# Performance work log

Hardware: AMD Instinct MI355X
Metric: run time of the kernel (lower is better)

Reference implementation:

```python
import jax, jax.numpy as jnp
import numpy as np

N_HEAD = 16


def setup_inputs() -> dict:
    key = jax.random.key(0)
    k1, k2, k3 = jax.random.split(key, 3)
    B, T, C = 2, 2048, 1024
    x = jax.random.normal(k1, (B, T, C), dtype=jnp.float32)
    w_attn = jax.random.normal(k2, (C, 3 * C), dtype=jnp.float32) * 0.02
    w_proj = jax.random.normal(k3, (C, C), dtype=jnp.float32) * 0.02
    return {"x": x, "w_attn": w_attn, "w_proj": w_proj}


def reference(x, w_attn, w_proj):
    B, T, C = x.shape
    H = N_HEAD
    D = C // H
    qkv = x @ w_attn  # [B, T, 3C]
    q, k, v = jnp.split(qkv, 3, axis=2)
    q = q.reshape(B, T, H, D)
    k = k.reshape(B, T, H, D)
    v = v.reshape(B, T, H, D)
    scale = 1.0 / jnp.sqrt(jnp.asarray(D, dtype=x.dtype))
    # Full T x T score matrix, matching the 'standard_attention' path.
    att = jnp.einsum('bthd,bshd->bhts', q, k) * scale  # [B, H, T, T]
    causal = jnp.tril(jnp.ones((T, T), dtype=bool))
    att = jnp.where(causal[None, None, :, :], att, jnp.asarray(-jnp.inf, dtype=att.dtype))
    att = jax.nn.softmax(att, axis=-1)
    # dropout_p is False (== 0.0) in the original module, so no dropout applied.
    y = jnp.einsum('bhts,bshd->bthd', att, v)  # [B, T, H, D]
    y = y.reshape(B, T, C)
    return y @ w_proj
```

## Files before the change

kernel.cpp:

```cpp
#include <hip/hip_runtime.h>
#include <hip/hip_bf16.h>
#include <math.h>

#define BB 2
#define TT 2048
#define HH 16
#define DD 64
#define CC 1024
#define C3 3072

typedef __attribute__((ext_vector_type(8))) short bf16x8;
typedef __attribute__((ext_vector_type(4))) short bf16x4;
typedef __attribute__((ext_vector_type(4))) float f32x4;
typedef __attribute__((ext_vector_type(2))) unsigned int u32x2;

__device__ __forceinline__ unsigned short f2bf(float f) {
  union { float f; unsigned u; } v; v.f = f;
  unsigned r = v.u + 0x7fffu + ((v.u >> 16) & 1u);
  return (unsigned short)(r >> 16);
}
__device__ __forceinline__ unsigned pack2bf(float a, float b) {
  __hip_bfloat162 h = __float22bfloat162_rn(make_float2(a, b));
  union { __hip_bfloat162 h; unsigned u; } cv; cv.h = h;
  return cv.u;
}

__device__ __forceinline__ void async_cp16(const void* g, void* l) {
  __builtin_amdgcn_global_load_lds(
      (const __attribute__((address_space(1))) void*)g,
      (__attribute__((address_space(3))) void*)l, 16, 0, 0);
}

__global__ __launch_bounds__(256)
void prep(const float* __restrict__ x, const float* __restrict__ w_attn,
          const float* __restrict__ w_proj, unsigned short* __restrict__ xb,
          unsigned short* __restrict__ wat, unsigned short* __restrict__ wpt) {
  __shared__ __align__(16) float Ts[64][68];
  const int bx = blockIdx.x, tid = threadIdx.x;
  if (bx < 1024) {
    int i = bx * 256 + tid;
#pragma unroll
    for (int it = 0; it < 4; ++it, i += 262144) {
      const float4 v = ((const float4*)x)[i];
      bf16x4 o = {(short)f2bf(v.x), (short)f2bf(v.y),
                  (short)f2bf(v.z), (short)f2bf(v.w)};
      ((bf16x4*)xb)[i] = o;
    }
    return;
  }
  const float* W;
  unsigned short* WT;
  int Nd, bound, n0, k0;
  float s;
  if (bx < 1792) {
    const int bid = bx - 1024;
    W = w_attn; WT = wat; Nd = 3072; bound = 1024; s = 0.18033688f;
    n0 = (bid % 48) * 64; k0 = (bid / 48) * 64;
  } else {
    const int bid = bx - 1792;
    W = w_proj; WT = wpt; Nd = 1024; bound = 0; s = 1.0f;
    n0 = (bid % 16) * 64; k0 = (bid / 16) * 64;
  }
  const int rl = tid >> 4, c4 = tid & 15;
#pragma unroll
  for (int it = 0; it < 4; ++it) {
    const int r = it * 16 + rl;
    *(float4*)&Ts[r][c4 * 4] =
        *(const float4*)(W + (size_t)(k0 + r) * Nd + n0 + c4 * 4);
  }
  __syncthreads();
#pragma unroll
  for (int it = 0; it < 4; ++it) {
    const int n = it * 16 + rl;
    const float sc = (n0 + n < bound) ? s : 1.0f;
    bf16x4 o = {(short)f2bf(Ts[c4 * 4 + 0][n] * sc),
                (short)f2bf(Ts[c4 * 4 + 1][n] * sc),
                (short)f2bf(Ts[c4 * 4 + 2][n] * sc),
                (short)f2bf(Ts[c4 * 4 + 3][n] * sc)};
    *(bf16x4*)(WT + (size_t)(n0 + n) * CC + k0 + c4 * 4) = o;
  }
}

__global__ __launch_bounds__(256, 3)
void gemm_qkv(const unsigned short* __restrict__ A,
              const unsigned short* __restrict__ BT,
              unsigned short* __restrict__ Cb,
              unsigned short* __restrict__ Vout) {
  __shared__ __align__(16) unsigned short As[2 * 128 * 32];
  __shared__ __align__(16) unsigned short Bs[2 * 128 * 32];

  const int tid = threadIdx.x;
  const int w = tid >> 6, lane = tid & 63;
  const int l15 = lane & 15, quad = lane >> 4;
  const int wm = w >> 1, wn = w & 1;
  const int row0 = blockIdx.y * 128, col0 = blockIdx.x * 128;

  const int ca0 = tid, ca1 = tid + 256;
  const int ra0 = ca0 >> 2, ka0 = ((ca0 & 3) ^ ((ca0 >> 3) & 3)) * 8;
  const int ra1 = ca1 >> 2, ka1 = ((ca1 & 3) ^ ((ca1 >> 3) & 3)) * 8;
  const unsigned short* gA0 = A + (size_t)(row0 + ra0) * CC + ka0;
  const unsigned short* gA1 = A + (size_t)(row0 + ra1) * CC + ka1;
  const unsigned short* gB0 = BT + (size_t)(col0 + ra0) * CC + ka0;
  const unsigned short* gB1 = BT + (size_t)(col0 + ra1) * CC + ka1;
  const int la0 = tid * 16, la1 = tid * 16 + 4096;

  const int fro = l15 * 64 + 16 * (quad ^ ((l15 >> 1) & 3));

  f32x4 acc[4][4];
#pragma unroll
  for (int i = 0; i < 4; ++i)
#pragma unroll
    for (int j = 0; j < 4; ++j) acc[i][j] = (f32x4){0.f, 0.f, 0.f, 0.f};

  async_cp16(gA0, (char*)As + la0);
  async_cp16(gA1, (char*)As + la1);
  async_cp16(gB0, (char*)Bs + la0);
  async_cp16(gB1, (char*)Bs + la1);

  for (int i = 0; i < 32; ++i) {
    const int cur = i & 1;
    __syncthreads();

    if (i + 1 < 32) {
      const int k1 = (i + 1) * 32;
      const int ab = (cur ^ 1) * 8192;
      async_cp16(gA0 + k1, (char*)As + ab + la0);
      async_cp16(gA1 + k1, (char*)As + ab + la1);
      async_cp16(gB0 + k1, (char*)Bs + ab + la0);
      async_cp16(gB1 + k1, (char*)Bs + ab + la1);
    }

    const char* fA = (const char*)As + cur * 8192 + wm * 4096 + fro;
    const char* fB = (const char*)Bs + cur * 8192 + wn * 4096 + fro;

    bf16x8 af[4], bf[4];
#pragma unroll
    for (int mt = 0; mt < 4; ++mt) af[mt] = *(const bf16x8*)(fA + mt * 1024);
#pragma unroll
    for (int nt = 0; nt < 4; ++nt) bf[nt] = *(const bf16x8*)(fB + nt * 1024);
#pragma unroll
    for (int mt = 0; mt < 4; ++mt)
#pragma unroll
      for (int nt = 0; nt < 4; ++nt)
        acc[mt][nt] = __builtin_amdgcn_mfma_f32_16x16x32_bf16(
            af[mt], bf[nt], acc[mt][nt], 0, 0, 0);
  }

  if (col0 >= 2048) {
#pragma unroll
    for (int mt = 0; mt < 4; ++mt) {
      const int rbase = row0 + wm * 64 + mt * 16 + quad * 4;
      const int bq = rbase >> 11, t0 = rbase & 2047;
#pragma unroll
      for (int nt = 0; nt < 4; ++nt) {
        const int d = col0 + wn * 64 + nt * 16 + l15 - 2048;
        bf16x4 o = {(short)f2bf(acc[mt][nt][0]), (short)f2bf(acc[mt][nt][1]),
                    (short)f2bf(acc[mt][nt][2]), (short)f2bf(acc[mt][nt][3])};
        *(bf16x4*)(Vout + (((size_t)(bq << 10) + d) << 11) + t0) = o;
      }
    }
  } else {
#pragma unroll
    for (int mt = 0; mt < 4; ++mt) {
      const int rbase = row0 + wm * 64 + mt * 16 + quad * 4;
#pragma unroll
      for (int r = 0; r < 4; ++r) {
        unsigned short* cr =
            Cb + (size_t)(rbase + r) * C3 + col0 + wn * 64 + l15;
#pragma unroll
        for (int nt = 0; nt < 4; ++nt) cr[nt * 16] = f2bf(acc[mt][nt][r]);
      }
    }
  }
}

__global__ __launch_bounds__(256, 2)
void gemm_out(const unsigned short* __restrict__ A,
              const unsigned short* __restrict__ BT,
              float* __restrict__ Cf) {
  __shared__ __align__(16) unsigned short As[2 * 64 * 64];
  __shared__ __align__(16) unsigned short Bs[2 * 128 * 64];

  const int tid = threadIdx.x;
  const int w = tid >> 6, lane = tid & 63;
  const int l15 = lane & 15, quad = lane >> 4;
  const int wm = w >> 1, wn = w & 1;
  const int row0 = blockIdx.y * 64, col0 = blockIdx.x * 128;

  const int ca0 = tid, ca1 = tid + 256;
  const int ra0 = ca0 >> 3, ka0 = ((ca0 & 7) ^ ((ca0 >> 3) & 7)) * 8;
  const int ra1 = ca1 >> 3, ka1 = ((ca1 & 7) ^ ((ca1 >> 3) & 7)) * 8;
  const unsigned short* gA0 = A + (size_t)(row0 + ra0) * CC + ka0;
  const unsigned short* gA1 = A + (size_t)(row0 + ra1) * CC + ka1;
  const unsigned short* gB[4];
  int lb[4];
#pragma unroll
  for (int t = 0; t < 4; ++t) {
    const int c = tid + t * 256;
    const int rb = c >> 3, kb = ((c & 7) ^ ((c >> 3) & 7)) * 8;
    gB[t] = BT + (size_t)(col0 + rb) * CC + kb;
    lb[t] = c * 16;
  }
  const int la0 = tid * 16, la1 = tid * 16 + 4096;

  const int fro = l15 * 128 + ((quad ^ (l15 & 7)) << 4);

  f32x4 acc[2][4];
#pragma unroll
  for (int i = 0; i < 2; ++i)
#pragma unroll
    for (int j = 0; j < 4; ++j) acc[i][j] = (f32x4){0.f, 0.f, 0.f, 0.f};

  async_cp16(gA0, (char*)As + la0);
  async_cp16(gA1, (char*)As + la1);
#pragma unroll
  for (int t = 0; t < 4; ++t) async_cp16(gB[t], (char*)Bs + lb[t]);

  for (int i = 0; i < 16; ++i) {
    const int cur = i & 1;
    __syncthreads();

    if (i + 1 < 16) {
      const int k1 = (i + 1) * 64;
      const int ab = (cur ^ 1) * 8192, bb = (cur ^ 1) * 16384;
      async_cp16(gA0 + k1, (char*)As + ab + la0);
      async_cp16(gA1 + k1, (char*)As + ab + la1);
#pragma unroll
      for (int t = 0; t < 4; ++t) async_cp16(gB[t] + k1, (char*)Bs + bb + lb[t]);
    }

    const char* fA = (const char*)As + cur * 8192 + wm * 4096 + fro;
    const char* fB = (const char*)Bs + cur * 16384 + wn * 8192 + fro;

#pragma unroll
    for (int kh = 0; kh < 2; ++kh) {
      const int xo = kh * 64;
      bf16x8 af[2], bf[4];
#pragma unroll
      for (int mt = 0; mt < 2; ++mt)
        af[mt] = *(const bf16x8*)(fA + mt * 2048 + ((fro + xo) & 127) - (fro & 127));
#pragma unroll
      for (int nt = 0; nt < 4; ++nt)
        bf[nt] = *(const bf16x8*)(fB + nt * 2048 + ((fro + xo) & 127) - (fro & 127));
#pragma unroll
      for (int mt = 0; mt < 2; ++mt)
#pragma unroll
        for (int nt = 0; nt < 4; ++nt)
          acc[mt][nt] = __builtin_amdgcn_mfma_f32_16x16x32_bf16(
              af[mt], bf[nt], acc[mt][nt], 0, 0, 0);
    }
  }

#pragma unroll
  for (int mt = 0; mt < 2; ++mt) {
    const int rbase = row0 + wm * 32 + mt * 16 + quad * 4;
#pragma unroll
    for (int r = 0; r < 4; ++r) {
      float* cr = Cf + (size_t)(rbase + r) * CC + col0 + wn * 64 + l15;
#pragma unroll
      for (int nt = 0; nt < 4; ++nt) cr[nt * 16] = acc[mt][nt][r];
    }
  }
}

__device__ __forceinline__ void attn_chunk(
    const int c, const int qt, const int l15, const int quad,
    const bf16x8 (&kf)[2][2], const bf16x8 (&qf)[4][2], const bf16x8 onesf,
    const unsigned short* __restrict__ vbase, char* psw, const int psrow,
    f32x4 (&O)[4][4], f32x4 (&lacc)[4]) {
  bf16x8 vf[4];
#pragma unroll
  for (int dt = 0; dt < 4; ++dt)
    vf[dt] = *(const bf16x8*)(vbase + (size_t)dt * 16 * TT + 32 * c);

  f32x4 S[2][4];
#pragma unroll
  for (int ks = 0; ks < 2; ++ks)
#pragma unroll
    for (int qs = 0; qs < 4; ++qs) {
      f32x4 z = (f32x4){-12.f, -12.f, -12.f, -12.f};
      z = __builtin_amdgcn_mfma_f32_16x16x32_bf16(kf[ks][0], qf[qs][0], z, 0, 0, 0);
      z = __builtin_amdgcn_mfma_f32_16x16x32_bf16(kf[ks][1], qf[qs][1], z, 0, 0, 0);
      S[ks][qs] = z;
    }

  if (c >= 2 * qt) {
#pragma unroll
    for (int ks = 0; ks < 2; ++ks)
#pragma unroll
      for (int qs = 0; qs < 4; ++qs)
#pragma unroll
        for (int r = 0; r < 4; ++r)
          if (32 * c + ks * 16 + quad * 4 + r > qt * 64 + qs * 16 + l15)
            S[ks][qs][r] = -INFINITY;
  }

#pragma unroll
  for (int ks = 0; ks < 2; ++ks)
#pragma unroll
    for (int qs = 0; qs < 4; ++qs) {
      u32x2 d;
      d[0] = pack2bf(__builtin_amdgcn_exp2f(S[ks][qs][0]),
                     __builtin_amdgcn_exp2f(S[ks][qs][1]));
      d[1] = pack2bf(__builtin_amdgcn_exp2f(S[ks][qs][2]),
                     __builtin_amdgcn_exp2f(S[ks][qs][3]));
      *(u32x2*)(psw + qs * 2304 + psrow + (((ks + l15) & 3) << 5) + quad * 8) = d;
    }

#pragma unroll
  for (int qs = 0; qs < 4; ++qs) {
    const bf16x8 pf = *(const bf16x8*)(psw + qs * 2304 + psrow +
                                       ((((quad >> 1) + l15) & 3) << 5) +
                                       ((quad & 1) << 4));
    lacc[qs] = __builtin_amdgcn_mfma_f32_16x16x32_bf16(onesf, pf, lacc[qs], 0, 0, 0);
#pragma unroll
    for (int dt = 0; dt < 4; ++dt)
      O[dt][qs] = __builtin_amdgcn_mfma_f32_16x16x32_bf16(vf[dt], pf, O[dt][qs], 0, 0, 0);
  }
}

#define LOADK(dst, cc)                                                   \
  do {                                                                   \
    const unsigned short* kp = kbase + (size_t)(32 * (cc)) * C3;         \
    dst[0][0] = *(const bf16x8*)(kp);                                    \
    dst[0][1] = *(const bf16x8*)(kp + 32);                               \
    dst[1][0] = *(const bf16x8*)(kp + 16 * C3);                          \
    dst[1][1] = *(const bf16x8*)(kp + 16 * C3 + 32);                     \
  } while (0)

__global__ __launch_bounds__(256, 2)
void attn_mfma(const unsigned short* __restrict__ qkvb,
               const unsigned short* __restrict__ vt,
               unsigned short* __restrict__ y) {
  const int n = blockIdx.x;
  const int bh = (n & 7) + 8 * ((n >> 3) & 3);
  const int qpair = n >> 5;
  const int b = bh >> 4, h = bh & 15;
  const int tid = threadIdx.x;
  const int w = tid >> 6;
  const int lane = tid & 63;
  const int l15 = lane & 15, quad = lane >> 4;

  __shared__ __align__(16) unsigned short Ps[4 * 4 * 16 * 72];
  __shared__ __align__(16) float Red[2][16][256];
  __shared__ float Red2[2][4][16];

  char* psw = (char*)Ps + w * (4 * 2304);
  const int psrow = l15 * 144;
  const int epoff = l15 * 64 + ((quad ^ (l15 & 3)) << 4);

  const unsigned short* kbase =
      qkvb + (size_t)(b * TT + l15) * C3 + 1024 + h * DD + quad * 8;
  const unsigned short* vbase =
      vt + (size_t)(bh * DD + l15) * TT + quad * 8;

  bf16x8 onesf;
#pragma unroll
  for (int jj = 0; jj < 8; ++jj) onesf[jj] = (short)0x3F80;

  for (int phase = 0; phase < 2; ++phase) {
    const int qt = phase ? qpair : 31 - qpair;
    const int nc = 2 * (qt + 1);

    const unsigned short* qbase =
        qkvb + (size_t)(b * TT + qt * 64 + l15) * C3 + h * DD + quad * 8;
    bf16x8 qf[4][2];
#pragma unroll
    for (int qs = 0; qs < 4; ++qs)
#pragma unroll
      for (int kh = 0; kh < 2; ++kh)
        qf[qs][kh] = *(const bf16x8*)(qbase + qs * 16 * C3 + kh * 32);

    f32x4 O[4][4];
    f32x4 lacc[4];
#pragma unroll
    for (int dt = 0; dt < 4; ++dt)
#pragma unroll
      for (int qs = 0; qs < 4; ++qs) O[dt][qs] = (f32x4){0.f, 0.f, 0.f, 0.f};
#pragma unroll
    for (int qs = 0; qs < 4; ++qs) lacc[qs] = (f32x4){0.f, 0.f, 0.f, 0.f};

    bf16x8 kfA[2][2], kfB[2][2];
    int c = w;
    if (c < nc) {
      LOADK(kfA, c);
      while (true) {
        int cn = c + 4;
        if (cn < nc) LOADK(kfB, cn);
        attn_chunk(c, qt, l15, quad, kfA, qf, onesf, vbase, psw, psrow, O, lacc);
        c = cn;
        if (c >= nc) break;
        cn = c + 4;
        if (cn < nc) LOADK(kfA, cn);
        attn_chunk(c, qt, l15, quad, kfB, qf, onesf, vbase, psw, psrow, O, lacc);
        c = cn;
        if (c >= nc) break;
      }
    }

    __syncthreads();
    if (w & 1) {
      char* rs = (char*)Red + (w >> 1) * 16384;
#pragma unroll
      for (int dt = 0; dt < 4; ++dt)
#pragma unroll
        for (int qs = 0; qs < 4; ++qs)
          *(f32x4*)(rs + (dt * 4 + qs) * 1024 + epoff) = O[dt][qs];
      if (quad == 0) {
#pragma unroll
        for (int qs = 0; qs < 4; ++qs) Red2[w >> 1][qs][l15] = lacc[qs][0];
      }
    }
    __syncthreads();
    float lsum[4];
#pragma unroll
    for (int qs = 0; qs < 4; ++qs) lsum[qs] = lacc[qs][0];
    if (!(w & 1)) {
      char* rs = (char*)Red + (w >> 1) * 16384;
#pragma unroll
      for (int dt = 0; dt < 4; ++dt)
#pragma unroll
        for (int qs = 0; qs < 4; ++qs)
          O[dt][qs] += *(const f32x4*)(rs + (dt * 4 + qs) * 1024 + epoff);
#pragma unroll
      for (int qs = 0; qs < 4; ++qs) lsum[qs] += Red2[w >> 1][qs][l15];
    }
    __syncthreads();
    if (w == 2) {
      char* rs = (char*)Red;
#pragma unroll
      for (int dt = 0; dt < 4; ++dt)
#pragma unroll
        for (int qs = 0; qs < 4; ++qs)
          *(f32x4*)(rs + (dt * 4 + qs) * 1024 + epoff) = O[dt][qs];
      if (quad == 0) {
#pragma unroll
        for (int qs = 0; qs < 4; ++qs) Red2[0][qs][l15] = lsum[qs];
      }
    }
    __syncthreads();
    if (w == 0) {
      char* rs = (char*)Red;
#pragma unroll
      for (int dt = 0; dt < 4; ++dt)
#pragma unroll
        for (int qs = 0; qs < 4; ++qs)
          O[dt][qs] += *(const f32x4*)(rs + (dt * 4 + qs) * 1024 + epoff);
      unsigned short* yr =
          y + (size_t)(b * TT + qt * 64 + l15) * CC + h * DD + quad * 4;
#pragma unroll
      for (int qs = 0; qs < 4; ++qs) {
        const float inv = 1.0f / (lsum[qs] + Red2[0][qs][l15]);
#pragma unroll
        for (int dt = 0; dt < 4; ++dt) {
          bf16x4 o = {(short)f2bf(O[dt][qs][0] * inv),
                      (short)f2bf(O[dt][qs][1] * inv),
                      (short)f2bf(O[dt][qs][2] * inv),
                      (short)f2bf(O[dt][qs][3] * inv)};
          *(bf16x4*)(yr + (size_t)qs * 16 * CC + dt * 16) = o;
        }
      }
    }
  }
}

extern "C" void kernel_launch(void* const* d_in, const int* in_sizes, int n_in,
                              void* d_out, int out_size, void* d_ws,
                              size_t ws_size, hipStream_t stream) {
  const float* x      = (const float*)d_in[0];
  const float* w_attn = (const float*)d_in[1];
  const float* w_proj = (const float*)d_in[2];
  float* out = (float*)d_out;

  unsigned short* xb   = (unsigned short*)d_ws;
  unsigned short* wat  = xb + (size_t)4096 * 1024;
  unsigned short* wpt  = wat + (size_t)3072 * 1024;
  unsigned short* qkvb = wpt + (size_t)1024 * 1024;
  unsigned short* vt   = qkvb + (size_t)4096 * 3072;
  unsigned short* yb   = vt + (size_t)BB * HH * DD * TT;

  dim3 blk(256);

  prep<<<2048, blk, 0, stream>>>(x, w_attn, w_proj, xb, wat, wpt);

  gemm_qkv<<<dim3(C3 / 128, (BB * TT) / 128), blk, 0, stream>>>(
      xb, wat, qkvb, vt);

  attn_mfma<<<dim3(512, 1, 1), blk, 0, stream>>>(qkvb, vt, yb);

  gemm_out<<<dim3(CC / 128, (BB * TT) / 64), blk, 0, stream>>>(yb, wpt, out);
}
```

Measured before the change: 173.8 us.

## Software-pipeline attention chunks: overlap next QK/exp with current PV MFMA

```diff
diff --git a/kernel.cpp b/kernel.cpp
--- a/kernel.cpp
+++ b/kernel.cpp
@@ -263,17 +263,10 @@
   }
 }
 
-__device__ __forceinline__ void attn_chunk(
+__device__ __forceinline__ void s_exp_pack(
     const int c, const int qt, const int l15, const int quad,
-    const bf16x8 (&kf)[2][2], const bf16x8 (&qf)[4][2], const bf16x8 onesf,
-    const unsigned short* __restrict__ vbase, char* psw, const int psrow,
-    f32x4 (&O)[4][4], f32x4 (&lacc)[4]) {
-  bf16x8 vf[4];
-#pragma unroll
-  for (int dt = 0; dt < 4; ++dt)
-    vf[dt] = *(const bf16x8*)(vbase + (size_t)dt * 16 * TT + 32 * c);
-
-  f32x4 S[2][4];
+    const bf16x8 (&kf)[2][2], const bf16x8 (&qf)[4][2],
+    unsigned (&P)[4][4]) {
 #pragma unroll
   for (int ks = 0; ks < 2; ++ks)
 #pragma unroll
@@ -281,32 +274,36 @@
       f32x4 z = (f32x4){-12.f, -12.f, -12.f, -12.f};
       z = __builtin_amdgcn_mfma_f32_16x16x32_bf16(kf[ks][0], qf[qs][0], z, 0, 0, 0);
       z = __builtin_amdgcn_mfma_f32_16x16x32_bf16(kf[ks][1], qf[qs][1], z, 0, 0, 0);
-      S[ks][qs] = z;
-    }
-
-  if (c >= 2 * qt) {
-#pragma unroll
-    for (int ks = 0; ks < 2; ++ks)
-#pragma unroll
-      for (int qs = 0; qs < 4; ++qs)
+      if (c >= 2 * qt) {
 #pragma unroll
         for (int r = 0; r < 4; ++r)
           if (32 * c + ks * 16 + quad * 4 + r > qt * 64 + qs * 16 + l15)
-            S[ks][qs][r] = -INFINITY;
-  }
-
+            z[r] = -INFINITY;
+      }
+      P[qs][2 * ks + 0] = pack2bf(__builtin_amdgcn_exp2f(z[0]),
+                                  __builtin_amdgcn_exp2f(z[1]));
+      P[qs][2 * ks + 1] = pack2bf(__builtin_amdgcn_exp2f(z[2]),
+                                  __builtin_amdgcn_exp2f(z[3]));
+    }
+}
+
+__device__ __forceinline__ void p_write(char* psw, const int psrow,
+                                        const int l15, const int quad,
+                                        const unsigned (&P)[4][4]) {
 #pragma unroll
   for (int ks = 0; ks < 2; ++ks)
 #pragma unroll
     for (int qs = 0; qs < 4; ++qs) {
-      u32x2 d;
-      d[0] = pack2bf(__builtin_amdgcn_exp2f(S[ks][qs][0]),
-                     __builtin_amdgcn_exp2f(S[ks][qs][1]));
-      d[1] = pack2bf(__builtin_amdgcn_exp2f(S[ks][qs][2]),
-                     __builtin_amdgcn_exp2f(S[ks][qs][3]));
+      u32x2 d = {P[qs][2 * ks + 0], P[qs][2 * ks + 1]};
       *(u32x2*)(psw + qs * 2304 + psrow + (((ks + l15) & 3) << 5) + quad * 8) = d;
     }
-
+}
+
+__device__ __forceinline__ void pv_accum(
+    const int l15, const int quad, const bf16x8 onesf,
+    const bf16x8 (&vf)[4], char* psw, const int psrow,
+    f32x4 (&O)[4][4], f32x4 (&lacc)[4]) {
+  __builtin_amdgcn_s_setprio(1);
 #pragma unroll
   for (int qs = 0; qs < 4; ++qs) {
     const bf16x8 pf = *(const bf16x8*)(psw + qs * 2304 + psrow +
@@ -317,6 +314,7 @@
     for (int dt = 0; dt < 4; ++dt)
       O[dt][qs] = __builtin_amdgcn_mfma_f32_16x16x32_bf16(vf[dt], pf, O[dt][qs], 0, 0, 0);
   }
+  __builtin_amdgcn_s_setprio(0);
 }
 
 #define LOADK(dst, cc)                                                   \
@@ -326,6 +324,15 @@
     dst[0][1] = *(const bf16x8*)(kp + 32);                               \
     dst[1][0] = *(const bf16x8*)(kp + 16 * C3);                          \
     dst[1][1] = *(const bf16x8*)(kp + 16 * C3 + 32);                     \
+  } while (0)
+
+#define LOADV(dst, cc)                                                   \
+  do {                                                                   \
+    const unsigned short* vp = vbase + 32 * (cc);                        \
+    dst[0] = *(const bf16x8*)(vp);                                       \
+    dst[1] = *(const bf16x8*)(vp + 16 * TT);                             \
+    dst[2] = *(const bf16x8*)(vp + 32 * TT);                             \
+    dst[3] = *(const bf16x8*)(vp + 48 * TT);                             \
   } while (0)
 
 __global__ __launch_bounds__(256, 2)
@@ -380,20 +387,28 @@
 #pragma unroll
     for (int qs = 0; qs < 4; ++qs) lacc[qs] = (f32x4){0.f, 0.f, 0.f, 0.f};
 
-    bf16x8 kfA[2][2], kfB[2][2];
     int c = w;
     if (c < nc) {
-      LOADK(kfA, c);
+      bf16x8 kX[2][2], kY[2][2], vf[4];
+      unsigned PX[4][4], PY[4][4];
+      LOADK(kX, c);
+      LOADV(vf, c);
+      if (c + 4 < nc) LOADK(kY, c + 4);
+      s_exp_pack(c, qt, l15, quad, kX, qf, PX);
       while (true) {
-        int cn = c + 4;
-        if (cn < nc) LOADK(kfB, cn);
-        attn_chunk(c, qt, l15, quad, kfA, qf, onesf, vbase, psw, psrow, O, lacc);
-        c = cn;
+        p_write(psw, psrow, l15, quad, PX);
+        if (c + 8 < nc) LOADK(kX, c + 8);
+        if (c + 4 < nc) s_exp_pack(c + 4, qt, l15, quad, kY, qf, PY);
+        pv_accum(l15, quad, onesf, vf, psw, psrow, O, lacc);
+        if (c + 4 < nc) LOADV(vf, c + 4);
+        c += 4;
         if (c >= nc) break;
-        cn = c + 4;
-        if (cn < nc) LOADK(kfA, cn);
-        attn_chunk(c, qt, l15, quad, kfB, qf, onesf, vbase, psw, psrow, O, lacc);
-        c = cn;
+        p_write(psw, psrow, l15, quad, PY);
+        if (c + 8 < nc) LOADK(kY, c + 8);
+        if (c + 4 < nc) s_exp_pack(c + 4, qt, l15, quad, kX, qf, PX);
+        pv_accum(l15, quad, onesf, vf, psw, psrow, O, lacc);
+        if (c + 4 < nc) LOADV(vf, c + 4);
+        c += 4;
         if (c >= nc) break;
       }
     }
```

Result: slower. 290.5 us (+67.1%).
